# Kernel optimization log

Hardware: AMD Instinct MI355X
Metric: run time of the kernel (lower is better)

Reference implementation:

```python
import jax, jax.numpy as jnp
import numpy as np

B, CIN, COUT, N, S, K, KS, DIM = 4, 64, 64, 32768, 8192, 32, 16, 3


def setup_inputs() -> dict:
    key = jax.random.key(0)
    ks = jax.random.split(key, 9)
    x = jax.random.normal(ks[0], (B, CIN, N), dtype=jnp.float32)
    pos = jax.random.normal(ks[1], (B, DIM, N), dtype=jnp.float32)
    support_points = jax.random.normal(ks[2], (B, DIM, S), dtype=jnp.float32)
    neighbors_indices = jax.random.randint(ks[3], (B, S, K), 0, N, dtype=jnp.int64)
    radius = jnp.ones((1,), dtype=jnp.float32)
    # learned params (Conv2d with 1x1 kernels == per-point matmuls)
    w_fc1 = jax.random.normal(ks[4], (KS, DIM), dtype=jnp.float32) * 0.1   # fc1: dim -> kernel_size
    w_fc2 = jax.random.normal(ks[5], (KS, 2 * KS), dtype=jnp.float32) * 0.1
    w_fc3 = jax.random.normal(ks[6], (KS, 2 * KS), dtype=jnp.float32) * 0.1
    w_cv = jax.random.normal(ks[7], (COUT, CIN, KS), dtype=jnp.float32) * 0.05  # Conv2d(CIN,COUT,(1,KS))
    return {"x": x, "pos": pos, "support_points": support_points,
            "neighbors_indices": neighbors_indices, "radius": radius,
            "w_fc1": w_fc1, "w_fc2": w_fc2, "w_fc3": w_fc3, "w_cv": w_cv}


def _gather(feat, idx):
    # feat: [B, C, N], idx: [B, S, K] -> [B, C, S, K]
    return jax.vmap(lambda f, i: f[:, i])(feat, idx)


def reference(x, pos, support_points, neighbors_indices, radius,
              w_fc1, w_fc2, w_fc3, w_cv):
    mask = (neighbors_indices > -1)                       # [B,S,K]
    idx = jnp.where(mask, neighbors_indices, 0)
    pos_g = _gather(pos, idx)                             # [B,3,S,K]
    x_g = _gather(x, idx)                                 # [B,CIN,S,K]

    pts = pos_g - support_points[..., None]               # [B,3,S,K]
    mask_pts = (~jnp.isinf(pts[:, :1])).astype(pts.dtype) # [B,1,S,K]
    pts = jnp.nan_to_num(pts, nan=0.0, posinf=0.0, neginf=0.0)
    pts = pts / radius[0]

    # distance weight: L2-normalize binary mask over neighbor axis (torch F.normalize, eps=1e-12)
    mf = mask.astype(pts.dtype)                           # [B,S,K]
    nrm = jnp.sqrt(jnp.sum(mf * mf, axis=2, keepdims=True))
    dw = (mf / jnp.maximum(nrm, 1e-12))[:, None]          # [B,1,S,K]
    dw = dw * mask_pts

    mat = jax.nn.relu(jnp.einsum('kd,bdsn->bksn', w_fc1, pts)) * dw
    mp1 = jnp.max(mat, axis=3, keepdims=True)
    mat = jnp.concatenate([mat, jnp.broadcast_to(mp1, mat.shape)], axis=1)
    mat = jax.nn.relu(jnp.einsum('km,bmsn->bksn', w_fc2, mat)) * dw
    mp2 = jnp.max(mat, axis=3, keepdims=True)
    mat = jnp.concatenate([mat, jnp.broadcast_to(mp2, mat.shape)], axis=1)
    mat = jax.nn.relu(jnp.einsum('km,bmsn->bksn', w_fc3, mat)) * dw    # [B,KS,S,K]

    # features[b,s,c,k] = sum_n x_g[b,c,s,n] * mat[b,k,s,n]
    feats = jnp.einsum('bcsn,bksn->bcsk', x_g, mat)        # [B,CIN,S,KS]
    out = jnp.einsum('ock,bcsk->bos', w_cv, feats)         # [B,COUT,S]

    sup_inf = jnp.isinf(support_points[:, :1, :])          # [B,1,S]
    out = jnp.where(sup_inf, jnp.inf, out)
    return out
```

## Files before the change

kernel.cpp:

```cpp
#include <hip/hip_runtime.h>
#include <math.h>

#define B_    4
#define CIN_  64
#define COUT_ 64
#define N_    32768
#define S_    8192

typedef __attribute__((ext_vector_type(8))) short short8;
typedef __attribute__((ext_vector_type(4))) float f32x4a;

static __device__ __forceinline__ unsigned short f2bf(float x) {
    unsigned u = __float_as_uint(x);
    u += 0x7fffu + ((u >> 16) & 1u);
    return (unsigned short)(u >> 16);
}
static __device__ __forceinline__ unsigned pack2bf(float a, float b) {
    return (unsigned)f2bf(a) | ((unsigned)f2bf(b) << 16);
}
template <int CTRL>
static __device__ __forceinline__ float max_ror(float v) {
    float r = __int_as_float(__builtin_amdgcn_update_dpp(
        __float_as_int(v), __float_as_int(v), CTRL, 0xf, 0xf, false));
    return fmaxf(v, r);
}
#define ROR8 0x128
#define ROR4 0x124
#define ROR2 0x122
#define ROR1 0x121

static __device__ __forceinline__ int fl(int p, int col) {
    return p * 2048 + (col ^ ((p & 7) << 4) ^ (((col >> 7) & 3) << 5));
}

__global__ __launch_bounds__(256) void transpose_x_kernel(
    const float* __restrict__ x, unsigned short* __restrict__ xTB)
{
    __shared__ float tile[64][65];
    const int b  = blockIdx.y;
    const int n0 = blockIdx.x * 64;
    const int tx = threadIdx.x & 63;
    const int ty = threadIdx.x >> 6;

    const float* xb = x + (size_t)b * CIN_ * N_;
    #pragma unroll
    for (int c = ty; c < 64; c += 4)
        tile[c][tx] = xb[(size_t)c * N_ + n0 + tx];
    __syncthreads();

    const int cp = threadIdx.x & 31;
    const int r0 = threadIdx.x >> 5;
    unsigned short* xTb = xTB + ((size_t)b * N_ + n0) * 64;
    #pragma unroll
    for (int nn = r0; nn < 64; nn += 8) {
        ushort2 v;
        v.x = f2bf(tile[2 * cp][nn]);
        v.y = f2bf(tile[2 * cp + 1][nn]);
        *(ushort2*)&xTb[(size_t)nn * 64 + 2 * cp] = v;
    }
}

__global__ __launch_bounds__(256) void post_kernel(
    const float* __restrict__ pos, float* __restrict__ posT)
{
    const int b = blockIdx.y;
    const int n = blockIdx.x * 256 + threadIdx.x;
    const float* pb = pos + (size_t)b * 3 * N_;
    float4 v = make_float4(pb[n], pb[N_ + n], pb[2 * N_ + n], 0.0f);
    *(float4*)&posT[((size_t)b * N_ + n) * 4] = v;
}

__global__ __launch_bounds__(256) void wcvb_kernel(
    const float* __restrict__ wcv, unsigned short* __restrict__ wcvB)
{
    const int i = blockIdx.x * 256 + threadIdx.x;
    const int o   = i >> 10;
    const int rem = i & 1023;
    const int k   = rem >> 6;
    const int c   = rem & 63;
    wcvB[i] = f2bf(wcv[(size_t)o * 1024 + c * 16 + k]);
}

__global__ __launch_bounds__(512) void fka_fused_kernel(
    const float* __restrict__ posT, const float* __restrict__ sup,
    const int*   __restrict__ nbr, const float* __restrict__ radius,
    const float* __restrict__ w1,  const float* __restrict__ w2,
    const float* __restrict__ w3,  const unsigned short* __restrict__ xTB,
    const unsigned short* __restrict__ wcvB,
    float* __restrict__ out)
{
    __shared__ unsigned short m3B[16 * 512];
    __shared__ unsigned short featsL[16 * 1024];
    __shared__ int   idxs[16][32];
    __shared__ float t2s[16][16];

    const int b  = blockIdx.y;
    const int t  = threadIdx.x;
    const int g  = t >> 5;
    const int n  = t & 31;
    const int s0 = blockIdx.x * 16;
    const int s  = s0 + g;

    const int raw    = nbr[(((size_t)b * S_ + s) << 5) + n];
    const bool valid = raw > -1;
    const int id     = valid ? raw : 0;

    unsigned long long bal = __ballot(valid);
    unsigned bits = (unsigned)(bal >> (t & 32));
    const float nrm = sqrtf((float)__popc(bits));
    float dw = valid ? (1.0f / fmaxf(nrm, 1e-12f)) : 0.0f;

    const float4 pg = *(const float4*)&posT[((size_t)b * N_ + id) * 4];
    float px = pg.x - sup[(size_t)(b * 3 + 0) * S_ + s];
    float py = pg.y - sup[(size_t)(b * 3 + 1) * S_ + s];
    float pz = pg.z - sup[(size_t)(b * 3 + 2) * S_ + s];
    if (isinf(px)) dw = 0.0f;
    px = (isnan(px) || isinf(px)) ? 0.0f : px;
    py = (isnan(py) || isinf(py)) ? 0.0f : py;
    pz = (isnan(pz) || isinf(pz)) ? 0.0f : pz;
    const float inv_r = 1.0f / radius[0];
    px *= inv_r; py *= inv_r; pz *= inv_r;

    const int kk = n & 15;

    float m1[16], mp1[16], m2[16], mp2[16], m3[16];

    #pragma unroll
    for (int k = 0; k < 16; ++k) {
        float v = w1[k * 3 + 0] * px + w1[k * 3 + 1] * py + w1[k * 3 + 2] * pz;
        m1[k] = fmaxf(v, 0.0f) * dw;
    }
    #pragma unroll
    for (int k = 0; k < 16; ++k) {
        float v = m1[k];
        v = fmaxf(v, __shfl_xor(v, 16, 32));
        v = max_ror<ROR8>(v); v = max_ror<ROR4>(v);
        v = max_ror<ROR2>(v); v = max_ror<ROR1>(v);
        mp1[k] = v;
    }
    {
        const float* wb = &w2[kk * 32 + 16];
        float pa = 0.0f, pb = 0.0f;
        #pragma unroll
        for (int j = 0; j < 8; ++j) pa = fmaf(wb[j], mp1[j], pa);
        #pragma unroll
        for (int j = 0; j < 8; ++j) pb = fmaf(wb[8 + j], mp1[8 + j], pb);
        float tp = (n & 16) ? pb : pa;
        tp += __shfl_xor(tp, 16, 32);
        t2s[g][kk] = tp;
    }
    {
        float4 ta = *(const float4*)&t2s[g][0];
        float4 tb = *(const float4*)&t2s[g][4];
        float4 tc = *(const float4*)&t2s[g][8];
        float4 td = *(const float4*)&t2s[g][12];
        float t2v[16] = {ta.x, ta.y, ta.z, ta.w, tb.x, tb.y, tb.z, tb.w,
                         tc.x, tc.y, tc.z, tc.w, td.x, td.y, td.z, td.w};
        #pragma unroll
        for (int k = 0; k < 16; ++k) {
            const float* wr = &w2[k * 32];
            float v = t2v[k];
            #pragma unroll
            for (int j = 0; j < 16; ++j) v = fmaf(wr[j], m1[j], v);
            m2[k] = fmaxf(v, 0.0f) * dw;
        }
    }
    #pragma unroll
    for (int k = 0; k < 16; ++k) {
        float v = m2[k];
        v = fmaxf(v, __shfl_xor(v, 16, 32));
        v = max_ror<ROR8>(v); v = max_ror<ROR4>(v);
        v = max_ror<ROR2>(v); v = max_ror<ROR1>(v);
        mp2[k] = v;
    }
    {
        const float* wb = &w3[kk * 32 + 16];
        float pa = 0.0f, pb = 0.0f;
        #pragma unroll
        for (int j = 0; j < 8; ++j) pa = fmaf(wb[j], mp2[j], pa);
        #pragma unroll
        for (int j = 0; j < 8; ++j) pb = fmaf(wb[8 + j], mp2[8 + j], pb);
        float tp = (n & 16) ? pb : pa;
        tp += __shfl_xor(tp, 16, 32);
        t2s[g][kk] = tp;
    }
    {
        float4 ta = *(const float4*)&t2s[g][0];
        float4 tb = *(const float4*)&t2s[g][4];
        float4 tc = *(const float4*)&t2s[g][8];
        float4 td = *(const float4*)&t2s[g][12];
        float t3v[16] = {ta.x, ta.y, ta.z, ta.w, tb.x, tb.y, tb.z, tb.w,
                         tc.x, tc.y, tc.z, tc.w, td.x, td.y, td.z, td.w};
        #pragma unroll
        for (int k = 0; k < 16; ++k) {
            const float* wr = &w3[k * 32];
            float v = t3v[k];
            #pragma unroll
            for (int j = 0; j < 16; ++j) v = fmaf(wr[j], m2[j], v);
            m3[k] = fmaxf(v, 0.0f) * dw;
        }
    }

    idxs[g][n] = id;
    {
        const int hi = n >> 3, jj = n & 7;
        unsigned short* base = &m3B[g * 512 + hi * 128 + jj];
        #pragma unroll
        for (int k = 0; k < 16; ++k) {
            const int row = (k + hi + g) & 15;
            base[row * 8] = f2bf(m3[k]);
        }
    }
    __syncthreads();

    const int wv  = t >> 6;
    const int l   = t & 63;
    const int hi2 = l >> 4;
    const int k15 = l & 15;
    const unsigned short* xb = xTB + (size_t)b * N_ * 64;
    char* fLp = (char*)featsL;

    for (int pp = 0; pp < 2; ++pp) {
        const int p = wv * 2 + pp;

        int ids8[8];
        #pragma unroll
        for (int j = 0; j < 8; ++j) ids8[j] = idxs[p][hi2 * 8 + j];

        const int brow = (k15 + hi2 + p) & 15;
        short8 bfrag = *(const short8*)&m3B[p * 512 + hi2 * 128 + brow * 8];

        f32x4a acc[4];
        #pragma unroll
        for (int ct = 0; ct < 4; ++ct) acc[ct] = (f32x4a){0.f, 0.f, 0.f, 0.f};

        #pragma unroll
        for (int ct = 0; ct < 4; ++ct) {
            union { unsigned short u[8]; short8 v; } A;
            #pragma unroll
            for (int j = 0; j < 8; ++j)
                A.u[j] = xb[((size_t)ids8[j] << 6) + ct * 16 + k15];
            acc[ct] = __builtin_amdgcn_mfma_f32_16x16x32_bf16(A.v, bfrag, acc[ct], 0, 0, 0);
        }

        #pragma unroll
        for (int ct = 0; ct < 4; ++ct) {
            uint2 val;
            val.x = pack2bf(acc[ct][0], acc[ct][1]);
            val.y = pack2bf(acc[ct][2], acc[ct][3]);
            const int col = k15 * 128 + ct * 32 + hi2 * 8;
            *(uint2*)(fLp + fl(p, col)) = val;
        }
    }
    __syncthreads();

    const int ot  = wv & 3;
    const int kh  = wv >> 2;
    const int lq  = hi2;
    const int l15 = k15;

    const unsigned short* apod =
        wcvB + (size_t)(ot * 16 + l15) * 1024 + kh * 512 + lq * 8;

    f32x4a oacc = (f32x4a){0.f, 0.f, 0.f, 0.f};
    #pragma unroll 4
    for (int ks = 0; ks < 16; ++ks) {
        const int col = kh * 1024 + ks * 64 + lq * 16;
        short8 bf = *(const short8*)(fLp + fl(l15, col));
        short8 af = *(const short8*)(apod + ks * 32);
        oacc = __builtin_amdgcn_mfma_f32_16x16x32_bf16(af, bf, oacc, 0, 0, 0);
    }

    float* pbuf = (float*)m3B;
    if (kh == 1) {
        #pragma unroll
        for (int r = 0; r < 4; ++r)
            pbuf[ot * 256 + (lq * 4 + r) * 16 + l15] = oacc[r];
    }
    __syncthreads();
    if (kh == 0) {
        const int sidx = s0 + l15;
        const bool infs = isinf(sup[(size_t)b * 3 * S_ + sidx]);
        #pragma unroll
        for (int r = 0; r < 4; ++r) {
            const float v = oacc[r] + pbuf[ot * 256 + (lq * 4 + r) * 16 + l15];
            const int o = ot * 16 + lq * 4 + r;
            out[((size_t)b * COUT_ + o) * S_ + sidx] = infs ? INFINITY : v;
        }
    }
}

extern "C" void kernel_launch(void* const* d_in, const int* in_sizes, int n_in,
                              void* d_out, int out_size, void* d_ws, size_t ws_size,
                              hipStream_t stream)
{
    const float* x   = (const float*)d_in[0];
    const float* pos = (const float*)d_in[1];
    const float* sup = (const float*)d_in[2];
    const int*   nbr = (const int*)d_in[3];
    const float* rad = (const float*)d_in[4];
    const float* w1  = (const float*)d_in[5];
    const float* w2  = (const float*)d_in[6];
    const float* w3  = (const float*)d_in[7];
    const float* wcv = (const float*)d_in[8];
    float* out = (float*)d_out;

    char* p = (char*)d_ws;
    unsigned short* xTB = (unsigned short*)p;  p += (size_t)B_ * N_ * 64 * sizeof(unsigned short);
    float* posT = (float*)p;                   p += (size_t)B_ * N_ * 4 * sizeof(float);
    unsigned short* wcvB = (unsigned short*)p; p += (size_t)COUT_ * 1024 * sizeof(unsigned short);

    transpose_x_kernel<<<dim3(N_ / 64, B_), 256, 0, stream>>>(x, xTB);
    post_kernel<<<dim3(N_ / 256, B_), 256, 0, stream>>>(pos, posT);
    wcvb_kernel<<<dim3(256), 256, 0, stream>>>(wcv, wcvB);

    fka_fused_kernel<<<dim3(S_ / 16, B_), 512, 0, stream>>>(
        posT, sup, nbr, rad, w1, w2, w3, xTB, wcvB, out);
}
```

Baseline: 80.80 us.

## Move fc2/fc3 per-point matmuls onto bf16 MFMA via shared-memory fragments

Replaces the scalar FMA loops for the fc2 and fc3 layers (16x16 per point) with bf16 MFMA instructions. m1 and m2 are staged through a swizzled shared buffer, and the max-pool reductions are restructured around the MFMA output layout. A small new kernel pre-packs the w2/w3 weight fragments into bf16. This cuts VALU work and register pressure, at the cost of bf16 rounding on intermediate activations and extra LDS traffic. The syncthreads between stages was also removed, which relies on each wave touching only its own data.

```diff
diff --git a/kernel.cpp b/kernel.cpp
--- a/kernel.cpp
+++ b/kernel.cpp
@@ -81,15 +81,31 @@
     wcvB[i] = f2bf(wcv[(size_t)o * 1024 + c * 16 + k]);
 }
 
+__global__ __launch_bounds__(128) void wfrag_kernel(
+    const float* __restrict__ w2, const float* __restrict__ w3,
+    unsigned short* __restrict__ wfr)
+{
+    const int t = threadIdx.x;
+    const int l = t & 63;
+    const float* w = (t >> 6) ? w3 : w2;
+    const int row = l & 15, hi = l >> 4;
+    #pragma unroll
+    for (int j = 0; j < 8; ++j) {
+        const int m = hi * 8 + j;
+        wfr[t * 8 + j] = (m < 16) ? f2bf(w[row * 32 + m]) : (unsigned short)0;
+    }
+}
+
 __global__ __launch_bounds__(512) void fka_fused_kernel(
     const float* __restrict__ posT, const float* __restrict__ sup,
     const int*   __restrict__ nbr, const float* __restrict__ radius,
     const float* __restrict__ w1,  const float* __restrict__ w2,
     const float* __restrict__ w3,  const unsigned short* __restrict__ xTB,
     const unsigned short* __restrict__ wcvB,
+    const unsigned short* __restrict__ wfr,
     float* __restrict__ out)
 {
-    __shared__ unsigned short m3B[16 * 512];
+    __shared__ unsigned short mbuf[16 * 512];
     __shared__ unsigned short featsL[16 * 1024];
     __shared__ int   idxs[16][32];
     __shared__ float t2s[16][16];
@@ -100,6 +116,10 @@
     const int n  = t & 31;
     const int s0 = blockIdx.x * 16;
     const int s  = s0 + g;
+    const int wv = t >> 6;
+    const int l  = t & 63;
+    const int l15 = l & 15;
+    const int hi  = l >> 4;
 
     const int raw    = nbr[(((size_t)b * S_ + s) << 5) + n];
     const bool valid = raw > -1;
@@ -121,15 +141,29 @@
     const float inv_r = 1.0f / radius[0];
     px *= inv_r; py *= inv_r; pz *= inv_r;
 
-    const int kk = n & 15;
-
-    float m1[16], mp1[16], m2[16], mp2[16], m3[16];
-
+    idxs[g][n] = id;
+
+    float m1[16];
     #pragma unroll
     for (int k = 0; k < 16; ++k) {
         float v = w1[k * 3 + 0] * px + w1[k * 3 + 1] * py + w1[k * 3 + 2] * pz;
         m1[k] = fmaxf(v, 0.0f) * dw;
     }
+
+    const int pp1 = g & 1, cg1 = n >> 4, col1 = n & 15;
+    {
+        const int base = wv * 1024 + pp1 * 512 + cg1 * 256;
+        const int swz  = ((col1 >> 2) & 3) << 3;
+        uint4 u0, u1;
+        u0.x = pack2bf(m1[0],  m1[1]);  u0.y = pack2bf(m1[2],  m1[3]);
+        u0.z = pack2bf(m1[4],  m1[5]);  u0.w = pack2bf(m1[6],  m1[7]);
+        u1.x = pack2bf(m1[8],  m1[9]);  u1.y = pack2bf(m1[10], m1[11]);
+        u1.z = pack2bf(m1[12], m1[13]); u1.w = pack2bf(m1[14], m1[15]);
+        *(uint4*)&mbuf[base + ((col1 * 16 + 0) ^ swz)] = u0;
+        *(uint4*)&mbuf[base + ((col1 * 16 + 8) ^ swz)] = u1;
+    }
+
+    float mp1[16];
     #pragma unroll
     for (int k = 0; k < 16; ++k) {
         float v = m1[k];
@@ -138,6 +172,8 @@
         v = max_ror<ROR2>(v); v = max_ror<ROR1>(v);
         mp1[k] = v;
     }
+
+    const int kk = n & 15;
     {
         const float* wb = &w2[kk * 32 + 16];
         float pa = 0.0f, pb = 0.0f;
@@ -149,74 +185,94 @@
         tp += __shfl_xor(tp, 16, 32);
         t2s[g][kk] = tp;
     }
+
+    const short8 aW2 = *(const short8*)(wfr + l * 8);
+    const short8 aW3 = *(const short8*)(wfr + 512 + l * 8);
+    const int swzr = ((l15 >> 2) & 3) << 3;
+
+    float mpm[2][4] = {{0.f,0.f,0.f,0.f},{0.f,0.f,0.f,0.f}};
+    #pragma unroll
+    for (int q = 0; q < 4; ++q) {
+        const int pp = q >> 1, cg = q & 1;
+        const int base = wv * 1024 + pp * 512 + cg * 256;
+        short8 bf = (short8){0,0,0,0,0,0,0,0};
+        if (hi < 2)
+            bf = *(const short8*)&mbuf[base + ((l15 * 16 + hi * 8) ^ swzr)];
+        f32x4a c = (f32x4a){0.f, 0.f, 0.f, 0.f};
+        c = __builtin_amdgcn_mfma_f32_16x16x32_bf16(aW2, bf, c, 0, 0, 0);
+        const float  dwq = __shfl(dw, pp * 32 + cg * 16 + l15, 64);
+        const float4 t2v = *(const float4*)&t2s[2 * wv + pp][hi * 4];
+        const float v0 = fmaxf(c[0] + t2v.x, 0.f) * dwq;
+        const float v1 = fmaxf(c[1] + t2v.y, 0.f) * dwq;
+        const float v2 = fmaxf(c[2] + t2v.z, 0.f) * dwq;
+        const float v3 = fmaxf(c[3] + t2v.w, 0.f) * dwq;
+        mpm[pp][0] = fmaxf(mpm[pp][0], v0);
+        mpm[pp][1] = fmaxf(mpm[pp][1], v1);
+        mpm[pp][2] = fmaxf(mpm[pp][2], v2);
+        mpm[pp][3] = fmaxf(mpm[pp][3], v3);
+        uint2 wval;
+        wval.x = pack2bf(v0, v1); wval.y = pack2bf(v2, v3);
+        *(uint2*)&mbuf[base + ((l15 * 16 + hi * 4) ^ swzr)] = wval;
+    }
+
+    #pragma unroll
+    for (int pp = 0; pp < 2; ++pp)
+        #pragma unroll
+        for (int r = 0; r < 4; ++r) {
+            float v = mpm[pp][r];
+            v = max_ror<ROR8>(v); v = max_ror<ROR4>(v);
+            v = max_ror<ROR2>(v); v = max_ror<ROR1>(v);
+            mpm[pp][r] = v;
+        }
+    if (l15 == 0) {
+        *(float4*)&t2s[2 * wv + 0][hi * 4] =
+            make_float4(mpm[0][0], mpm[0][1], mpm[0][2], mpm[0][3]);
+        *(float4*)&t2s[2 * wv + 1][hi * 4] =
+            make_float4(mpm[1][0], mpm[1][1], mpm[1][2], mpm[1][3]);
+    }
+
     {
-        float4 ta = *(const float4*)&t2s[g][0];
-        float4 tb = *(const float4*)&t2s[g][4];
-        float4 tc = *(const float4*)&t2s[g][8];
-        float4 td = *(const float4*)&t2s[g][12];
-        float t2v[16] = {ta.x, ta.y, ta.z, ta.w, tb.x, tb.y, tb.z, tb.w,
-                         tc.x, tc.y, tc.z, tc.w, td.x, td.y, td.z, td.w};
-        #pragma unroll
-        for (int k = 0; k < 16; ++k) {
-            const float* wr = &w2[k * 32];
-            float v = t2v[k];
-            #pragma unroll
-            for (int j = 0; j < 16; ++j) v = fmaf(wr[j], m1[j], v);
-            m2[k] = fmaxf(v, 0.0f) * dw;
-        }
-    }
-    #pragma unroll
-    for (int k = 0; k < 16; ++k) {
-        float v = m2[k];
-        v = fmaxf(v, __shfl_xor(v, 16, 32));
-        v = max_ror<ROR8>(v); v = max_ror<ROR4>(v);
-        v = max_ror<ROR2>(v); v = max_ror<ROR1>(v);
-        mp2[k] = v;
-    }
-    {
-        const float* wb = &w3[kk * 32 + 16];
-        float pa = 0.0f, pb = 0.0f;
-        #pragma unroll
-        for (int j = 0; j < 8; ++j) pa = fmaf(wb[j], mp2[j], pa);
-        #pragma unroll
-        for (int j = 0; j < 8; ++j) pb = fmaf(wb[8 + j], mp2[8 + j], pb);
-        float tp = (n & 16) ? pb : pa;
-        tp += __shfl_xor(tp, 16, 32);
-        t2s[g][kk] = tp;
-    }
-    {
-        float4 ta = *(const float4*)&t2s[g][0];
-        float4 tb = *(const float4*)&t2s[g][4];
-        float4 tc = *(const float4*)&t2s[g][8];
-        float4 td = *(const float4*)&t2s[g][12];
-        float t3v[16] = {ta.x, ta.y, ta.z, ta.w, tb.x, tb.y, tb.z, tb.w,
-                         tc.x, tc.y, tc.z, tc.w, td.x, td.y, td.z, td.w};
-        #pragma unroll
-        for (int k = 0; k < 16; ++k) {
-            const float* wr = &w3[k * 32];
-            float v = t3v[k];
-            #pragma unroll
-            for (int j = 0; j < 16; ++j) v = fmaf(wr[j], m2[j], v);
-            m3[k] = fmaxf(v, 0.0f) * dw;
-        }
-    }
-
-    idxs[g][n] = id;
-    {
-        const int hi = n >> 3, jj = n & 7;
-        unsigned short* base = &m3B[g * 512 + hi * 128 + jj];
-        #pragma unroll
-        for (int k = 0; k < 16; ++k) {
-            const int row = (k + hi + g) & 15;
-            base[row * 8] = f2bf(m3[k]);
-        }
-    }
-    __syncthreads();
-
-    const int wv  = t >> 6;
-    const int l   = t & 63;
-    const int hi2 = l >> 4;
-    const int k15 = l & 15;
+        const int pz = l >> 5;
+        const float4 ma  = *(const float4*)&t2s[2 * wv + pz][0];
+        const float4 mb2 = *(const float4*)&t2s[2 * wv + pz][4];
+        const float4 mc  = *(const float4*)&t2s[2 * wv + pz][8];
+        const float4 md  = *(const float4*)&t2s[2 * wv + pz][12];
+        const float mp2v[16] = {ma.x, ma.y, ma.z, ma.w, mb2.x, mb2.y, mb2.z, mb2.w,
+                                mc.x, mc.y, mc.z, mc.w, md.x, md.y, md.z, md.w};
+        const float* wb3 = &w3[(l & 15) * 32 + 16];
+        float t3 = 0.0f;
+        #pragma unroll
+        for (int m = 0; m < 16; ++m) t3 = fmaf(wb3[m], mp2v[m], t3);
+        t2s[2 * wv + pz][l & 15] = t3;
+    }
+
+    #pragma unroll
+    for (int q = 0; q < 4; ++q) {
+        const int pp = q >> 1, cg = q & 1;
+        const int p  = 2 * wv + pp;
+        const int base = wv * 1024 + pp * 512 + cg * 256;
+        short8 bf = (short8){0,0,0,0,0,0,0,0};
+        if (hi < 2)
+            bf = *(const short8*)&mbuf[base + ((l15 * 16 + hi * 8) ^ swzr)];
+        f32x4a c = (f32x4a){0.f, 0.f, 0.f, 0.f};
+        c = __builtin_amdgcn_mfma_f32_16x16x32_bf16(aW3, bf, c, 0, 0, 0);
+        const float  dwq = __shfl(dw, pp * 32 + cg * 16 + l15, 64);
+        const float4 t3v = *(const float4*)&t2s[p][hi * 4];
+        const float v0 = fmaxf(c[0] + t3v.x, 0.f) * dwq;
+        const float v1 = fmaxf(c[1] + t3v.y, 0.f) * dwq;
+        const float v2 = fmaxf(c[2] + t3v.z, 0.f) * dwq;
+        const float v3 = fmaxf(c[3] + t3v.w, 0.f) * dwq;
+        const int nn = cg * 16 + l15;
+        const int hh = nn >> 3, jj = nn & 7;
+        unsigned short* wb = &mbuf[p * 512 + hh * 128 + jj];
+        wb[(((hi * 4 + 0) + hh + p) & 15) * 8] = f2bf(v0);
+        wb[(((hi * 4 + 1) + hh + p) & 15) * 8] = f2bf(v1);
+        wb[(((hi * 4 + 2) + hh + p) & 15) * 8] = f2bf(v2);
+        wb[(((hi * 4 + 3) + hh + p) & 15) * 8] = f2bf(v3);
+    }
+
+    const int hi2 = hi;
+    const int k15 = l15;
     const unsigned short* xb = xTB + (size_t)b * N_ * 64;
     char* fLp = (char*)featsL;
 
@@ -228,7 +284,7 @@
         for (int j = 0; j < 8; ++j) ids8[j] = idxs[p][hi2 * 8 + j];
 
         const int brow = (k15 + hi2 + p) & 15;
-        short8 bfrag = *(const short8*)&m3B[p * 512 + hi2 * 128 + brow * 8];
+        short8 bfrag = *(const short8*)&mbuf[p * 512 + hi2 * 128 + brow * 8];
 
         f32x4a acc[4];
         #pragma unroll
@@ -254,10 +310,9 @@
     }
     __syncthreads();
 
-    const int ot  = wv & 3;
-    const int kh  = wv >> 2;
-    const int lq  = hi2;
-    const int l15 = k15;
+    const int ot = wv & 3;
+    const int kh = wv >> 2;
+    const int lq = hi2;
 
     const unsigned short* apod =
         wcvB + (size_t)(ot * 16 + l15) * 1024 + kh * 512 + lq * 8;
@@ -266,12 +321,12 @@
     #pragma unroll 4
     for (int ks = 0; ks < 16; ++ks) {
         const int col = kh * 1024 + ks * 64 + lq * 16;
-        short8 bf = *(const short8*)(fLp + fl(l15, col));
-        short8 af = *(const short8*)(apod + ks * 32);
-        oacc = __builtin_amdgcn_mfma_f32_16x16x32_bf16(af, bf, oacc, 0, 0, 0);
-    }
-
-    float* pbuf = (float*)m3B;
+        short8 bfv = *(const short8*)(fLp + fl(l15, col));
+        short8 afv = *(const short8*)(apod + ks * 32);
+        oacc = __builtin_amdgcn_mfma_f32_16x16x32_bf16(afv, bfv, oacc, 0, 0, 0);
+    }
+
+    float* pbuf = (float*)mbuf;
     if (kh == 1) {
         #pragma unroll
         for (int r = 0; r < 4; ++r)
@@ -309,11 +364,13 @@
     unsigned short* xTB = (unsigned short*)p;  p += (size_t)B_ * N_ * 64 * sizeof(unsigned short);
     float* posT = (float*)p;                   p += (size_t)B_ * N_ * 4 * sizeof(float);
     unsigned short* wcvB = (unsigned short*)p; p += (size_t)COUT_ * 1024 * sizeof(unsigned short);
+    unsigned short* wfr = (unsigned short*)p;  p += (size_t)2 * 64 * 8 * sizeof(unsigned short);
 
     transpose_x_kernel<<<dim3(N_ / 64, B_), 256, 0, stream>>>(x, xTB);
     post_kernel<<<dim3(N_ / 256, B_), 256, 0, stream>>>(pos, posT);
     wcvb_kernel<<<dim3(256), 256, 0, stream>>>(wcv, wcvB);
+    wfrag_kernel<<<dim3(1), 128, 0, stream>>>(w2, w3, wfr);
 
     fka_fused_kernel<<<dim3(S_ / 16, B_), 512, 0, stream>>>(
-        posT, sup, nbr, rad, w1, w2, w3, xTB, wcvB, out);
-}
+        posT, sup, nbr, rad, w1, w2, w3, xTB, wcvB, wfr, out);
+}
```

After: 86.70 us. 1.07x slower.
